# Optimization experiments

Measured on AMD Instinct MI355X. Metric: run time of the kernel, lower is better.

Reference implementation:

```python
import jax, jax.numpy as jnp
import numpy as np

T = 4          # spiking time steps
HEADS = 12
SCALE = 0.125
TAU = 2.0
ALPHA = 4.0    # sigmoid surrogate sharpness
EPS = 1e-5

@jax.custom_vjp
def spike(x):
    # Heaviside forward, sigmoid surrogate backward (SigmoidGrad)
    return (x > 0).astype(x.dtype)

def _spike_fwd(x):
    return (x > 0).astype(x.dtype), x

def _spike_bwd(x, g):
    s = jax.nn.sigmoid(ALPHA * x)
    return (g * ALPHA * s * (1.0 - s),)

spike.defvjp(_spike_fwd, _spike_bwd)

def lif(x, threshold):
    # layer-by-layer LIF: x is [T*B, ...]; scan membrane over T steps
    TB = x.shape[0]
    B = TB // T
    xt = x.reshape((T, B) + x.shape[1:])
    def step(mem, xi):
        mem = mem + (xi - mem) / TAU
        s = spike(mem - threshold)
        mem = mem * (1.0 - jax.lax.stop_gradient(s))  # hard reset, spike detached
        return mem, s
    _, sp = jax.lax.scan(step, jnp.zeros_like(xt[0]), xt)
    return sp.reshape(x.shape)

def bn(x, p):
    # inference BatchNorm; p = [gamma, beta, mean, var] each [C], channel axis 1
    shape = (1, x.shape[1]) + (1,) * (x.ndim - 2)
    inv = jax.lax.rsqrt(p[3] + EPS)
    return (x - p[2].reshape(shape)) * (p[0] * inv).reshape(shape) + p[1].reshape(shape)

def setup_inputs() -> dict:
    key = jax.random.key(0)
    ks = jax.random.split(key, 9)
    C, HID, TB, H = 384, 1536, 128, 14
    return {
        'x': jax.random.normal(ks[0], (TB, C, H, H), jnp.float32),
        'qkvp_w': jax.random.normal(ks[1], (4, C, C), jnp.float32) * 0.05,
        'qkvp_bn': jax.random.uniform(ks[2], (4, 4, C), jnp.float32),
        'fc1_w': jax.random.normal(ks[3], (HID, C), jnp.float32) * 0.05,
        'fc1_b': jax.random.normal(ks[4], (HID,), jnp.float32) * 0.05,
        'fc1_bn': jax.random.uniform(ks[5], (4, HID), jnp.float32),
        'fc2_w': jax.random.normal(ks[6], (C, HID), jnp.float32) * 0.05,
        'fc2_b': jax.random.normal(ks[7], (C,), jnp.float32) * 0.05,
        'fc2_bn': jax.random.uniform(ks[8], (4, C), jnp.float32),
    }

def reference(x, qkvp_w, qkvp_bn, fc1_w, fc1_b, fc1_bn, fc2_w, fc2_b, fc2_bn):
    TB, C, H, W = x.shape
    N = H * W
    d = C // HEADS
    xf = x.reshape(TB, C, N)

    def branch(i):
        y = jnp.einsum('oc,bcn->bon', qkvp_w[i], xf)  # conv1d k=1, no bias
        y = lif(bn(y, qkvp_bn[i]), 1.0)
        # [TB,C,N] -> [TB,N,C] -> [TB,N,heads,d] -> [TB,heads,N,d]
        return y.transpose(0, 2, 1).reshape(TB, N, HEADS, d).transpose(0, 2, 1, 3)

    q, k, v = branch(0), branch(1), branch(2)
    attn = jnp.einsum('bhqd,bhkd->bhqk', q, k) * SCALE  # no softmax (spiking SSA)
    o = jnp.einsum('bhqk,bhkd->bhqd', attn, v)
    o = o.transpose(0, 1, 3, 2).reshape(TB, C, N)       # head-major channel layout
    o = lif(o, 0.5)                                     # attn_lif threshold=0.5
    o = jnp.einsum('oc,bcn->bon', qkvp_w[3], o)         # proj conv
    o = lif(bn(o, qkvp_bn[3]), 1.0).reshape(TB, C, H, W)

    x = x + o                                           # attention residual

    h = jnp.einsum('oc,bchw->bohw', fc1_w, x) + fc1_b[None, :, None, None]
    h = lif(bn(h, fc1_bn), 1.0)
    h = jnp.einsum('oc,bchw->bohw', fc2_w, h) + fc2_b[None, :, None, None]
    h = lif(bn(h, fc2_bn), 1.0)

    x = x + h                                           # MLP residual
    return (x, v)
```

## Files before the change

### kernel.cpp

```cpp
#include <hip/hip_runtime.h>
#include <hip/hip_bf16.h>


#define Cv 384
#define Nv 196
#define Mv 25088
#define HIDv 1536
#define Bv 32
#define Zv 6272
#define TBv 128

__global__ __launch_bounds__(256) void k_transpose_in(const float* __restrict__ x,
                                                      float* __restrict__ xp)
{
    int idx = blockIdx.x * 256 + threadIdx.x;
    int c   = idx / Mv;
    int rem = idx - c * Mv;
    int z = rem >> 2, t = rem & 3;
    int b = z / Nv, n = z - b * Nv;
    xp[idx] = x[((size_t)(t * Bv + b) * Cv + c) * Nv + n];
}

template<int XBF16, int SADD, int BIAS, int EPI>
__global__ __launch_bounds__(256) void k_gemm5(const float* __restrict__ W,
                                               const void* __restrict__ Xv,
                                               const __hip_bfloat16* __restrict__ Xs,
                                               const float* __restrict__ bias,
                                               const float* __restrict__ bnp,
                                               int bnC,
                                               void* __restrict__ Y,
                                               int K, int NO)
{
    __shared__ float sX[8][256];
    int id    = blockIdx.x;
    int chunk = gridDim.x >> 3;
    int idp   = (id & 7) * chunk + (id >> 3);
    int m0    = (idp / NO) * 256;
    int obt   = idp % NO;
    int tid  = threadIdx.x;
    int lane = tid & 63;
    int wid  = __builtin_amdgcn_readfirstlane(tid >> 6);
    int ob   = obt * 32 + wid * 8;
    int mL   = m0 + lane * 4;
    int r1   = tid >> 6;
    int c1   = (tid & 63) * 4;

    float acc[8][4];
    #pragma unroll
    for (int i = 0; i < 8; ++i)
        #pragma unroll
        for (int j = 0; j < 4; ++j) acc[i][j] = 0.0f;

    for (int k0 = 0; k0 < K; k0 += 8) {
        float xfa[4], xfb[4];
        if (XBF16) {
            const unsigned short* Xb = (const unsigned short*)Xv;
            uint2 ua = *(const uint2*)(Xb + (size_t)(k0 + r1) * Mv + m0 + c1);
            uint2 ub = *(const uint2*)(Xb + (size_t)(k0 + r1 + 4) * Mv + m0 + c1);
            xfa[0] = __uint_as_float((ua.x & 0xFFFFu) << 16);
            xfa[1] = __uint_as_float(ua.x & 0xFFFF0000u);
            xfa[2] = __uint_as_float((ua.y & 0xFFFFu) << 16);
            xfa[3] = __uint_as_float(ua.y & 0xFFFF0000u);
            xfb[0] = __uint_as_float((ub.x & 0xFFFFu) << 16);
            xfb[1] = __uint_as_float(ub.x & 0xFFFF0000u);
            xfb[2] = __uint_as_float((ub.y & 0xFFFFu) << 16);
            xfb[3] = __uint_as_float(ub.y & 0xFFFF0000u);
        } else {
            const float* Xf = (const float*)Xv;
            float4 xa = *(const float4*)(Xf + (size_t)(k0 + r1) * Mv + m0 + c1);
            float4 xb = *(const float4*)(Xf + (size_t)(k0 + r1 + 4) * Mv + m0 + c1);
            xfa[0]=xa.x; xfa[1]=xa.y; xfa[2]=xa.z; xfa[3]=xa.w;
            xfb[0]=xb.x; xfb[1]=xb.y; xfb[2]=xb.z; xfb[3]=xb.w;
            if (SADD) {
                const unsigned short* Sb = (const unsigned short*)Xs;
                uint2 ua = *(const uint2*)(Sb + (size_t)(k0 + r1) * Mv + m0 + c1);
                uint2 ub = *(const uint2*)(Sb + (size_t)(k0 + r1 + 4) * Mv + m0 + c1);
                xfa[0] = __fadd_rn(xfa[0], (ua.x & 0xFFFFu)      ? 1.0f : 0.0f);
                xfa[1] = __fadd_rn(xfa[1], (ua.x & 0xFFFF0000u) ? 1.0f : 0.0f);
                xfa[2] = __fadd_rn(xfa[2], (ua.y & 0xFFFFu)      ? 1.0f : 0.0f);
                xfa[3] = __fadd_rn(xfa[3], (ua.y & 0xFFFF0000u) ? 1.0f : 0.0f);
                xfb[0] = __fadd_rn(xfb[0], (ub.x & 0xFFFFu)      ? 1.0f : 0.0f);
                xfb[1] = __fadd_rn(xfb[1], (ub.x & 0xFFFF0000u) ? 1.0f : 0.0f);
                xfb[2] = __fadd_rn(xfb[2], (ub.y & 0xFFFFu)      ? 1.0f : 0.0f);
                xfb[3] = __fadd_rn(xfb[3], (ub.y & 0xFFFF0000u) ? 1.0f : 0.0f);
            }
        }
        __syncthreads();
        *(float4*)&sX[r1][c1]     = *(float4*)&xfa[0];
        *(float4*)&sX[r1 + 4][c1] = *(float4*)&xfb[0];
        __syncthreads();
        const float* Wb = W + (size_t)ob * K + k0;
        #pragma unroll
        for (int kk = 0; kk < 8; ++kk) {
            float4 xq = *(const float4*)&sX[kk][lane * 4];
            float xv[4] = {xq.x, xq.y, xq.z, xq.w};
            #pragma unroll
            for (int i = 0; i < 8; ++i) {
                float wv = Wb[(size_t)i * K + kk];
                #pragma unroll
                for (int j = 0; j < 4; ++j)
                    acc[i][j] = fmaf(wv, xv[j], acc[i][j]);
            }
        }
    }

    #pragma unroll
    for (int i = 0; i < 8; ++i) {
        int o = ob + i;
        if (EPI == 0) {
            float bb = BIAS ? bias[o] : 0.0f;
            float4 r;
            r.x = acc[i][0] + bb; r.y = acc[i][1] + bb;
            r.z = acc[i][2] + bb; r.w = acc[i][3] + bb;
            *(float4*)((float*)Y + (size_t)o * Mv + mL) = r;
        } else {
            float inv = __fdiv_rn(1.0f, __fsqrt_rn(__fadd_rn(bnp[3*bnC + o], 1e-5f)));
            float scl = __fmul_rn(bnp[o], inv);
            float mu  = bnp[2*bnC + o];
            float be  = bnp[bnC + o];
            float mem = 0.0f;
            ushort4 pk;
            unsigned short* pks = (unsigned short*)&pk;
            #pragma unroll
            for (int j = 0; j < 4; ++j) {
                float val = acc[i][j];
                if (BIAS) val = __fadd_rn(val, bias[o]);
                float bn = __fadd_rn(__fmul_rn(__fsub_rn(val, mu), scl), be);
                mem = __fadd_rn(mem, __fmul_rn(__fsub_rn(bn, mem), 0.5f));
                int s = (mem > 1.0f);
                mem = s ? 0.0f : mem;
                pks[j] = s ? 0x3F80 : 0;
            }
            *(ushort4*)((unsigned short*)Y + (size_t)o * Mv + mL) = pk;
        }
    }
}

__global__ __launch_bounds__(256) void k_vsse2(const float* __restrict__ W,
                                               const float* __restrict__ X,
                                               const float* __restrict__ bnp,
                                               __hip_bfloat16* __restrict__ Y)
{
    __shared__ float sW[32][68];
    __shared__ float sX[32][64];
    int id    = blockIdx.x;
    int chunk = gridDim.x >> 3;
    int idp   = (id & 7) * chunk + (id >> 3);
    int m0    = (idp / 6) * 64;
    int o0    = (idp % 6) * 64;
    int tid = threadIdx.x;
    int to = tid >> 4, tm = tid & 15;

    float acc[4][4][4];
    #pragma unroll
    for (int s = 0; s < 4; ++s)
        #pragma unroll
        for (int op = 0; op < 4; ++op)
            #pragma unroll
            for (int e = 0; e < 4; ++e) acc[s][op][e] = 0.0f;

    int wq_o = tid >> 3, wq_c = tid & 7;
    int xs_r = tid >> 3, xs_c = (tid & 7) * 8;

    for (int blk = 0; blk < 12; ++blk) {
        int k0 = blk * 32;
        __syncthreads();
        {
            float4 w4 = *(const float4*)(W + (size_t)(o0 + wq_o) * Cv + k0 + wq_c*4);
            sW[wq_c*4+0][wq_o] = w4.x;
            sW[wq_c*4+1][wq_o] = w4.y;
            sW[wq_c*4+2][wq_o] = w4.z;
            sW[wq_c*4+3][wq_o] = w4.w;
            float4 w5 = *(const float4*)(W + (size_t)(o0 + 32 + wq_o) * Cv + k0 + wq_c*4);
            sW[wq_c*4+0][32 + wq_o] = w5.x;
            sW[wq_c*4+1][32 + wq_o] = w5.y;
            sW[wq_c*4+2][32 + wq_o] = w5.z;
            sW[wq_c*4+3][32 + wq_o] = w5.w;
        }
        {
            const float* Xp = X + (size_t)(k0 + xs_r) * Mv + m0 + xs_c;
            *(float4*)&sX[xs_r][xs_c]     = *(const float4*)(Xp);
            *(float4*)&sX[xs_r][xs_c + 4] = *(const float4*)(Xp + 4);
        }
        __syncthreads();
        #pragma unroll
        for (int j = 0; j < 8; ++j) {
            #pragma unroll
            for (int s = 0; s < 4; ++s) {
                int kk = j * 4 + s;
                float4 w4 = *(const float4*)&sW[kk][to*4];
                float4 x4 = *(const float4*)&sX[kk][tm*4];
                float wv[4] = {w4.x, w4.y, w4.z, w4.w};
                float xv[4] = {x4.x, x4.y, x4.z, x4.w};
                #pragma unroll
                for (int op = 0; op < 4; ++op)
                    #pragma unroll
                    for (int e = 0; e < 4; ++e)
                        acc[s][op][e] = __fadd_rn(acc[s][op][e],
                                                  __fmul_rn(wv[op], xv[e]));
            }
        }
    }

    #pragma unroll
    for (int op = 0; op < 4; ++op) {
        int o = o0 + to*4 + op;
        float inv = __fdiv_rn(1.0f, __fsqrt_rn(__fadd_rn(bnp[3*Cv + o], 1e-5f)));
        float sc  = __fmul_rn(bnp[o], inv);
        float mu  = bnp[2*Cv + o];
        float be  = bnp[Cv + o];
        float mem = 0.0f;
        ushort4 pk;
        unsigned short* pks = (unsigned short*)&pk;
        #pragma unroll
        for (int e = 0; e < 4; ++e) {
            float tot = __fadd_rn(__fadd_rn(acc[0][op][e], acc[2][op][e]),
                                  __fadd_rn(acc[1][op][e], acc[3][op][e]));
            float bn = __fadd_rn(__fmul_rn(__fsub_rn(tot, mu), sc), be);
            mem = __fadd_rn(mem, __fmul_rn(__fsub_rn(bn, mem), 0.5f));
            int s = (mem > 1.0f);
            mem = s ? 0.0f : mem;
            pks[e] = s ? 0x3F80 : 0;
        }
        *(ushort4*)((unsigned short*)Y + (size_t)o * Mv + m0 + tm * 4) = pk;
    }
}

__global__ __launch_bounds__(256) void k_attn(const __hip_bfloat16* __restrict__ qs,
                                              const __hip_bfloat16* __restrict__ ks,
                                              const __hip_bfloat16* __restrict__ vs,
                                              float* __restrict__ o_chan,
                                              float* __restrict__ v_out)
{
    int h = blockIdx.x, tbl = blockIdx.y;
    int t = tbl >> 5, b = tbl & 31;
    int tid = threadIdx.x;
    __shared__ unsigned kmask[196];
    __shared__ float vf[196][36];
    size_t chb  = (size_t)h * 32 * Mv;
    size_t colb = (size_t)b * Nv * 4 + t;

    for (int e = tid; e < Nv * 32; e += 256) {
        int dd = e / Nv, n = e - dd * Nv;
        vf[n][dd] = __bfloat162float(vs[chb + (size_t)dd * Mv + colb + (size_t)n * 4]);
    }
    unsigned qm = 0;
    if (tid < Nv) {
        unsigned km = 0;
        #pragma unroll
        for (int dd = 0; dd < 32; ++dd) {
            size_t off = chb + (size_t)dd * Mv + colb + (size_t)tid * 4;
            km |= (__bfloat162float(ks[off]) > 0.5f ? 1u : 0u) << dd;
            qm |= (__bfloat162float(qs[off]) > 0.5f ? 1u : 0u) << dd;
        }
        kmask[tid] = km;
    }
    __syncthreads();
    for (int e = tid; e < Nv * 32; e += 256) {
        int n = e >> 5, dd = e & 31;
        v_out[((size_t)(tbl * 12 + h) * Nv + n) * 32 + dd] = vf[n][dd];
    }
    if (tid < Nv) {
        float acc[32] = {};
        for (int nk = 0; nk < Nv; ++nk) {
            float a = (float)__popc(qm & kmask[nk]) * 0.125f;
            #pragma unroll
            for (int dd = 0; dd < 32; ++dd) acc[dd] += a * vf[nk][dd];
        }
        #pragma unroll
        for (int dd = 0; dd < 32; ++dd)
            o_chan[chb + (size_t)dd * Mv + colb + (size_t)tid * 4] = acc[dd];
    }
}

__global__ __launch_bounds__(256) void k_attnlif(float* __restrict__ o)
{
    int idx = blockIdx.x * 256 + threadIdx.x;
    size_t base = (size_t)idx * 4;
    float4 v = *(const float4*)(o + base);
    float xi[4] = {v.x, v.y, v.z, v.w};
    float s4[4];
    float mem = 0.f;
    #pragma unroll
    for (int t = 0; t < 4; ++t) {
        mem = mem + (xi[t] - mem) * 0.5f;
        s4[t] = (mem > 0.5f) ? 1.0f : 0.0f;
        mem *= (1.0f - s4[t]);
    }
    float4 r; r.x = s4[0]; r.y = s4[1]; r.z = s4[2]; r.w = s4[3];
    *(float4*)(o + base) = r;
}

__global__ __launch_bounds__(256) void k_final(const float* __restrict__ h2,
                                               const float* __restrict__ bnp,
                                               const float* __restrict__ x,
                                               const __hip_bfloat16* __restrict__ s_proj,
                                               float* __restrict__ out)
{
    int idx = blockIdx.x * 256 + threadIdx.x;
    int c = idx / Zv;
    int z = idx - c * Zv;
    int b = z / Nv, n = z - b * Nv;
    float gamma = bnp[c], beta = bnp[Cv+c], mean = bnp[2*Cv+c], var = bnp[3*Cv+c];
    float scale = gamma / sqrtf(var + 1e-5f);
    size_t base = (size_t)idx * 4;
    float4 hv = *(const float4*)(h2 + base);
    float xi[4] = {hv.x, hv.y, hv.z, hv.w};
    ushort4 sp4 = *(const ushort4*)((const unsigned short*)s_proj + base);
    unsigned short* sps = (unsigned short*)&sp4;
    float mem = 0.f;
    #pragma unroll
    for (int t = 0; t < 4; ++t) {
        float bnv = (xi[t] - mean) * scale + beta;
        mem = mem + (bnv - mem) * 0.5f;
        float s = (mem > 1.0f) ? 1.0f : 0.0f;
        mem *= (1.0f - s);
        size_t oidx = ((size_t)(t * Bv + b) * Cv + c) * Nv + n;
        float sproj = sps[t] ? 1.0f : 0.0f;
        out[oidx] = x[oidx] + sproj + s;
    }
}

extern "C" void kernel_launch(void* const* d_in, const int* in_sizes, int n_in,
                              void* d_out, int out_size, void* d_ws, size_t ws_size,
                              hipStream_t stream)
{
    const float* x       = (const float*)d_in[0];
    const float* qkvp_w  = (const float*)d_in[1];
    const float* qkvp_bn = (const float*)d_in[2];
    const float* fc1_w   = (const float*)d_in[3];
    const float* fc1_b   = (const float*)d_in[4];
    const float* fc1_bn  = (const float*)d_in[5];
    const float* fc2_w   = (const float*)d_in[6];
    const float* fc2_b   = (const float*)d_in[7];
    const float* fc2_bn  = (const float*)d_in[8];

    float* out1 = (float*)d_out;
    float* out2 = out1 + (size_t)TBv * Cv * Nv;

    const size_t S  = (size_t)Cv * Mv;
    const size_t S4 = S * 4;
    if (ws_size < 4 * S4) return;

    char* wb = (char*)d_ws;
    float* xp            = (float*)wb;
    float* obuf          = (float*)(wb + S4);
    __hip_bfloat16* qs   = (__hip_bfloat16*)(wb + 2*S4);
    __hip_bfloat16* ks   = (__hip_bfloat16*)(wb + 2*S4 + S4/2);
    __hip_bfloat16* vs   = (__hip_bfloat16*)(wb + 3*S4);
    __hip_bfloat16* s_pr = (__hip_bfloat16*)(wb + 3*S4 + S4/2);
    __hip_bfloat16* H    = (__hip_bfloat16*)(wb + S4);
    float* h2            = (float*)wb;

    k_transpose_in<<<(int)(S/256), 256, 0, stream>>>(x, xp);

    k_gemm5<0,0,0,1><<<1176, 256, 0, stream>>>(
        qkvp_w, xp, nullptr, nullptr, qkvp_bn, Cv, qs, Cv, 12);
    k_gemm5<0,0,0,1><<<1176, 256, 0, stream>>>(
        qkvp_w + (size_t)Cv*Cv, xp, nullptr, nullptr, qkvp_bn + 4*Cv, Cv, ks, Cv, 12);
    k_vsse2<<<2352, 256, 0, stream>>>(qkvp_w + (size_t)2*Cv*Cv, xp,
                                      qkvp_bn + (size_t)2*4*Cv, vs);

    k_attn<<<dim3(12, 128), 256, 0, stream>>>(qs, ks, vs, obuf, out2);
    k_attnlif<<<(int)(S/1024), 256, 0, stream>>>(obuf);

    k_gemm5<0,0,0,1><<<1176, 256, 0, stream>>>(
        qkvp_w + (size_t)3*Cv*Cv, obuf, nullptr, nullptr, qkvp_bn + 3*4*Cv, Cv, s_pr, Cv, 12);

    k_gemm5<0,1,1,1><<<4704, 256, 0, stream>>>(
        fc1_w, xp, s_pr, fc1_b, fc1_bn, HIDv, H, Cv, 48);

    k_gemm5<1,0,1,0><<<1176, 256, 0, stream>>>(
        fc2_w, H, nullptr, fc2_b, nullptr, 0, h2, HIDv, 12);

    k_final<<<(int)(S/1024), 256, 0, stream>>>(h2, fc2_bn, x, s_pr, out1);
}
```

Measured before the change: 1.193 ms.

## Fuse Q and K projection GEMMs and deepen K-tile to 16

Merges the separate Q and K projection GEMM launches into one kernel that reads each staged X tile once and accumulates both outputs, halving X traffic for these two branches. The shared GEMM kernel's K-step also doubles from 8 to 16, so there are fewer barriers per K element. The price is twice as many accumulator registers in the fused kernel, which can lower occupancy, and a larger shared-memory tile.

```diff
diff --git a/kernel.cpp b/kernel.cpp
--- a/kernel.cpp
+++ b/kernel.cpp
@@ -19,6 +19,54 @@
     int z = rem >> 2, t = rem & 3;
     int b = z / Nv, n = z - b * Nv;
     xp[idx] = x[((size_t)(t * Bv + b) * Cv + c) * Nv + n];
+}
+
+template<int XBF16, int SADD>
+__device__ __forceinline__ void g5_row(const void* __restrict__ Xv,
+                                       const __hip_bfloat16* __restrict__ Xs,
+                                       int row, int c1, int m0, float* xf)
+{
+    if (XBF16) {
+        const unsigned short* Xb = (const unsigned short*)Xv;
+        uint2 u = *(const uint2*)(Xb + (size_t)row * Mv + m0 + c1);
+        xf[0] = __uint_as_float((u.x & 0xFFFFu) << 16);
+        xf[1] = __uint_as_float(u.x & 0xFFFF0000u);
+        xf[2] = __uint_as_float((u.y & 0xFFFFu) << 16);
+        xf[3] = __uint_as_float(u.y & 0xFFFF0000u);
+    } else {
+        const float* Xf = (const float*)Xv;
+        float4 xa = *(const float4*)(Xf + (size_t)row * Mv + m0 + c1);
+        xf[0]=xa.x; xf[1]=xa.y; xf[2]=xa.z; xf[3]=xa.w;
+        if (SADD) {
+            const unsigned short* Sb = (const unsigned short*)Xs;
+            uint2 u = *(const uint2*)(Sb + (size_t)row * Mv + m0 + c1);
+            xf[0] = __fadd_rn(xf[0], (u.x & 0xFFFFu)      ? 1.0f : 0.0f);
+            xf[1] = __fadd_rn(xf[1], (u.x & 0xFFFF0000u) ? 1.0f : 0.0f);
+            xf[2] = __fadd_rn(xf[2], (u.y & 0xFFFFu)      ? 1.0f : 0.0f);
+            xf[3] = __fadd_rn(xf[3], (u.y & 0xFFFF0000u) ? 1.0f : 0.0f);
+        }
+    }
+}
+
+__device__ __forceinline__ void g5_epi_spike(const float* acc4, const float* bias,
+                                             const float* bnp, int bnC, int o,
+                                             int BIAS, unsigned short* pks)
+{
+    float inv = __fdiv_rn(1.0f, __fsqrt_rn(__fadd_rn(bnp[3*bnC + o], 1e-5f)));
+    float scl = __fmul_rn(bnp[o], inv);
+    float mu  = bnp[2*bnC + o];
+    float be  = bnp[bnC + o];
+    float mem = 0.0f;
+    #pragma unroll
+    for (int j = 0; j < 4; ++j) {
+        float val = acc4[j];
+        if (BIAS) val = __fadd_rn(val, bias[o]);
+        float bn = __fadd_rn(__fmul_rn(__fsub_rn(val, mu), scl), be);
+        mem = __fadd_rn(mem, __fmul_rn(__fsub_rn(bn, mem), 0.5f));
+        int s = (mem > 1.0f);
+        mem = s ? 0.0f : mem;
+        pks[j] = s ? 0x3F80 : 0;
+    }
 }
 
 template<int XBF16, int SADD, int BIAS, int EPI>
@@ -31,16 +79,15 @@
                                                void* __restrict__ Y,
                                                int K, int NO)
 {
-    __shared__ float sX[8][256];
+    __shared__ float sX[16][256];
     int id    = blockIdx.x;
     int chunk = gridDim.x >> 3;
     int idp   = (id & 7) * chunk + (id >> 3);
     int m0    = (idp / NO) * 256;
-    int obt   = idp % NO;
     int tid  = threadIdx.x;
     int lane = tid & 63;
     int wid  = __builtin_amdgcn_readfirstlane(tid >> 6);
-    int ob   = obt * 32 + wid * 8;
+    int ob   = (idp % NO) * 32 + wid * 8;
     int mL   = m0 + lane * 4;
     int r1   = tid >> 6;
     int c1   = (tid & 63) * 4;
@@ -51,47 +98,19 @@
         #pragma unroll
         for (int j = 0; j < 4; ++j) acc[i][j] = 0.0f;
 
-    for (int k0 = 0; k0 < K; k0 += 8) {
-        float xfa[4], xfb[4];
-        if (XBF16) {
-            const unsigned short* Xb = (const unsigned short*)Xv;
-            uint2 ua = *(const uint2*)(Xb + (size_t)(k0 + r1) * Mv + m0 + c1);
-            uint2 ub = *(const uint2*)(Xb + (size_t)(k0 + r1 + 4) * Mv + m0 + c1);
-            xfa[0] = __uint_as_float((ua.x & 0xFFFFu) << 16);
-            xfa[1] = __uint_as_float(ua.x & 0xFFFF0000u);
-            xfa[2] = __uint_as_float((ua.y & 0xFFFFu) << 16);
-            xfa[3] = __uint_as_float(ua.y & 0xFFFF0000u);
-            xfb[0] = __uint_as_float((ub.x & 0xFFFFu) << 16);
-            xfb[1] = __uint_as_float(ub.x & 0xFFFF0000u);
-            xfb[2] = __uint_as_float((ub.y & 0xFFFFu) << 16);
-            xfb[3] = __uint_as_float(ub.y & 0xFFFF0000u);
-        } else {
-            const float* Xf = (const float*)Xv;
-            float4 xa = *(const float4*)(Xf + (size_t)(k0 + r1) * Mv + m0 + c1);
-            float4 xb = *(const float4*)(Xf + (size_t)(k0 + r1 + 4) * Mv + m0 + c1);
-            xfa[0]=xa.x; xfa[1]=xa.y; xfa[2]=xa.z; xfa[3]=xa.w;
-            xfb[0]=xb.x; xfb[1]=xb.y; xfb[2]=xb.z; xfb[3]=xb.w;
-            if (SADD) {
-                const unsigned short* Sb = (const unsigned short*)Xs;
-                uint2 ua = *(const uint2*)(Sb + (size_t)(k0 + r1) * Mv + m0 + c1);
-                uint2 ub = *(const uint2*)(Sb + (size_t)(k0 + r1 + 4) * Mv + m0 + c1);
-                xfa[0] = __fadd_rn(xfa[0], (ua.x & 0xFFFFu)      ? 1.0f : 0.0f);
-                xfa[1] = __fadd_rn(xfa[1], (ua.x & 0xFFFF0000u) ? 1.0f : 0.0f);
-                xfa[2] = __fadd_rn(xfa[2], (ua.y & 0xFFFFu)      ? 1.0f : 0.0f);
-                xfa[3] = __fadd_rn(xfa[3], (ua.y & 0xFFFF0000u) ? 1.0f : 0.0f);
-                xfb[0] = __fadd_rn(xfb[0], (ub.x & 0xFFFFu)      ? 1.0f : 0.0f);
-                xfb[1] = __fadd_rn(xfb[1], (ub.x & 0xFFFF0000u) ? 1.0f : 0.0f);
-                xfb[2] = __fadd_rn(xfb[2], (ub.y & 0xFFFFu)      ? 1.0f : 0.0f);
-                xfb[3] = __fadd_rn(xfb[3], (ub.y & 0xFFFF0000u) ? 1.0f : 0.0f);
-            }
-        }
-        __syncthreads();
-        *(float4*)&sX[r1][c1]     = *(float4*)&xfa[0];
-        *(float4*)&sX[r1 + 4][c1] = *(float4*)&xfb[0];
+    for (int k0 = 0; k0 < K; k0 += 16) {
+        float xf[4][4];
+        #pragma unroll
+        for (int qq = 0; qq < 4; ++qq)
+            g5_row<XBF16, SADD>(Xv, Xs, k0 + r1 + qq*4, c1, m0, xf[qq]);
+        __syncthreads();
+        #pragma unroll
+        for (int qq = 0; qq < 4; ++qq)
+            *(float4*)&sX[r1 + qq*4][c1] = *(float4*)&xf[qq][0];
         __syncthreads();
         const float* Wb = W + (size_t)ob * K + k0;
         #pragma unroll
-        for (int kk = 0; kk < 8; ++kk) {
+        for (int kk = 0; kk < 16; ++kk) {
             float4 xq = *(const float4*)&sX[kk][lane * 4];
             float xv[4] = {xq.x, xq.y, xq.z, xq.w};
             #pragma unroll
@@ -114,25 +133,76 @@
             r.z = acc[i][2] + bb; r.w = acc[i][3] + bb;
             *(float4*)((float*)Y + (size_t)o * Mv + mL) = r;
         } else {
-            float inv = __fdiv_rn(1.0f, __fsqrt_rn(__fadd_rn(bnp[3*bnC + o], 1e-5f)));
-            float scl = __fmul_rn(bnp[o], inv);
-            float mu  = bnp[2*bnC + o];
-            float be  = bnp[bnC + o];
-            float mem = 0.0f;
             ushort4 pk;
-            unsigned short* pks = (unsigned short*)&pk;
+            g5_epi_spike(acc[i], bias, bnp, bnC, o, BIAS, (unsigned short*)&pk);
+            *(ushort4*)((unsigned short*)Y + (size_t)o * Mv + mL) = pk;
+        }
+    }
+}
+
+__global__ __launch_bounds__(256) void k_gemmqk(const float* __restrict__ Wq,
+                                                const float* __restrict__ Wk,
+                                                const float* __restrict__ X,
+                                                const float* __restrict__ bnp,
+                                                __hip_bfloat16* __restrict__ Yq,
+                                                __hip_bfloat16* __restrict__ Yk)
+{
+    __shared__ float sX[16][256];
+    int id    = blockIdx.x;
+    int chunk = gridDim.x >> 3;
+    int idp   = (id & 7) * chunk + (id >> 3);
+    int m0    = (idp / 12) * 256;
+    int tid  = threadIdx.x;
+    int lane = tid & 63;
+    int wid  = __builtin_amdgcn_readfirstlane(tid >> 6);
+    int ob   = (idp % 12) * 32 + wid * 8;
+    int mL   = m0 + lane * 4;
+    int r1   = tid >> 6;
+    int c1   = (tid & 63) * 4;
+
+    float accq[8][4], acck[8][4];
+    #pragma unroll
+    for (int i = 0; i < 8; ++i)
+        #pragma unroll
+        for (int j = 0; j < 4; ++j) { accq[i][j] = 0.0f; acck[i][j] = 0.0f; }
+
+    for (int k0 = 0; k0 < Cv; k0 += 16) {
+        float xf[4][4];
+        #pragma unroll
+        for (int qq = 0; qq < 4; ++qq)
+            g5_row<0,0>(X, nullptr, k0 + r1 + qq*4, c1, m0, xf[qq]);
+        __syncthreads();
+        #pragma unroll
+        for (int qq = 0; qq < 4; ++qq)
+            *(float4*)&sX[r1 + qq*4][c1] = *(float4*)&xf[qq][0];
+        __syncthreads();
+        const float* Wqb = Wq + (size_t)ob * Cv + k0;
+        const float* Wkb = Wk + (size_t)ob * Cv + k0;
+        #pragma unroll
+        for (int kk = 0; kk < 16; ++kk) {
+            float4 xq = *(const float4*)&sX[kk][lane * 4];
+            float xv[4] = {xq.x, xq.y, xq.z, xq.w};
             #pragma unroll
-            for (int j = 0; j < 4; ++j) {
-                float val = acc[i][j];
-                if (BIAS) val = __fadd_rn(val, bias[o]);
-                float bn = __fadd_rn(__fmul_rn(__fsub_rn(val, mu), scl), be);
-                mem = __fadd_rn(mem, __fmul_rn(__fsub_rn(bn, mem), 0.5f));
-                int s = (mem > 1.0f);
-                mem = s ? 0.0f : mem;
-                pks[j] = s ? 0x3F80 : 0;
+            for (int i = 0; i < 8; ++i) {
+                float wq = Wqb[(size_t)i * Cv + kk];
+                float wk = Wkb[(size_t)i * Cv + kk];
+                #pragma unroll
+                for (int j = 0; j < 4; ++j) {
+                    accq[i][j] = fmaf(wq, xv[j], accq[i][j]);
+                    acck[i][j] = fmaf(wk, xv[j], acck[i][j]);
+                }
             }
-            *(ushort4*)((unsigned short*)Y + (size_t)o * Mv + mL) = pk;
-        }
+        }
+    }
+
+    #pragma unroll
+    for (int i = 0; i < 8; ++i) {
+        int o = ob + i;
+        ushort4 pkq, pkk;
+        g5_epi_spike(accq[i], nullptr, bnp,          Cv, o, 0, (unsigned short*)&pkq);
+        g5_epi_spike(acck[i], nullptr, bnp + 4*Cv,   Cv, o, 0, (unsigned short*)&pkk);
+        *(ushort4*)((unsigned short*)Yq + (size_t)o * Mv + mL) = pkq;
+        *(ushort4*)((unsigned short*)Yk + (size_t)o * Mv + mL) = pkk;
     }
 }
 
@@ -354,10 +424,8 @@
 
     k_transpose_in<<<(int)(S/256), 256, 0, stream>>>(x, xp);
 
-    k_gemm5<0,0,0,1><<<1176, 256, 0, stream>>>(
-        qkvp_w, xp, nullptr, nullptr, qkvp_bn, Cv, qs, Cv, 12);
-    k_gemm5<0,0,0,1><<<1176, 256, 0, stream>>>(
-        qkvp_w + (size_t)Cv*Cv, xp, nullptr, nullptr, qkvp_bn + 4*Cv, Cv, ks, Cv, 12);
+    k_gemmqk<<<1176, 256, 0, stream>>>(qkvp_w, qkvp_w + (size_t)Cv*Cv, xp,
+                                       qkvp_bn, qs, ks);
     k_vsse2<<<2352, 256, 0, stream>>>(qkvp_w + (size_t)2*Cv*Cv, xp,
                                       qkvp_bn + (size_t)2*4*Cv, vs);
 
```

Measured after the change: 1.515 ms. 27.0% more time.
